# Optimization experiments

Measured on AMD Instinct MI355X. Metric: run time of the kernel, lower is better.

Reference implementation:

```python
import jax, jax.numpy as jnp
import numpy as np
import math

B, S, D, H = 4, 2048, 1024, 16
HD = D // H

def setup_inputs() -> dict:
    key = jax.random.key(0)
    ks = jax.random.split(key, 14)
    scale = 1.0 / math.sqrt(D)
    inp = {
        "q": jax.random.normal(ks[0], (B, S, D), jnp.float32),
        "k": jax.random.normal(ks[1], (B, S, D), jnp.float32),
        "v": jax.random.normal(ks[2], (B, S, D), jnp.float32),
        "time_diffs": jax.random.uniform(ks[3], (B, S, S), jnp.float32),
        "mask": jax.random.randint(ks[4], (B, 1, S, S), 0, 2, jnp.int32),
        "Wq": jax.random.normal(ks[5], (D, D), jnp.float32) * scale,
        "bq": jnp.zeros((D,), jnp.float32),
        "Wk": jax.random.normal(ks[6], (D, D), jnp.float32) * scale,
        "bk": jnp.zeros((D,), jnp.float32),
        "Wv": jax.random.normal(ks[7], (D, D), jnp.float32) * scale,
        "bv": jnp.zeros((D,), jnp.float32),
        "Wo": jax.random.normal(ks[8], (D, D), jnp.float32) * scale,
        "bo": jnp.zeros((D,), jnp.float32),
        "gamma": jnp.asarray(1.0, jnp.float32),
    }
    return inp


def reference(q, k, v, time_diffs, mask, Wq, bq, Wk, bk, Wv, bv, Wo, bo, gamma):
    # Linear projections (torch Linear: x @ W.T + b), split heads -> [B,H,S,HD]
    def proj(x, W, b):
        return (x @ W.T + b).reshape(B, S, H, HD).transpose(0, 2, 1, 3)

    qh = proj(q, Wq, bq)
    kh = proj(k, Wk, bk)
    vh = proj(v, Wv, bv)

    # [B,H,S,S] attention scores
    scores = jnp.einsum("bhqd,bhkd->bhqk", qh, kh) / math.sqrt(HD)
    # additive time-decay bias, broadcast over heads
    scores = scores + jnp.exp(-gamma * time_diffs)[:, None, :, :]
    scores = jnp.where(mask == 0, jnp.float32(-1e9), scores)

    attn = jax.nn.softmax(scores, axis=-1)
    # dropout is identity in eval mode (training=False)
    out = jnp.einsum("bhqk,bhkd->bhqd", attn, vh)
    out = out.transpose(0, 2, 1, 3).reshape(B, S, D)
    return out @ Wo.T + bo
```

## Files before the change

### kernel.cpp

```cpp
#include <hip/hip_runtime.h>
#include <hip/hip_bf16.h>

#define B_ 4
#define S_ 2048
#define D_ 1024
#define H_ 16
#define M_ 8192

typedef __attribute__((ext_vector_type(8))) _Float16 h8;
typedef __attribute__((ext_vector_type(4))) _Float16 h4;
typedef __attribute__((ext_vector_type(8))) short    s8;
typedef __attribute__((ext_vector_type(4))) float    f4;

#define AS1(p) ((const __attribute__((address_space(1))) void*)(p))
#define AS3(p) ((__attribute__((address_space(3))) void*)(p))

__device__ __forceinline__ f4 mfma16(h8 a, h8 b, f4 c) {
  return __builtin_amdgcn_mfma_f32_16x16x32_f16(a, b, c, 0, 0, 0);
}

struct CastArgs {
  const float* src[7];
  _Float16*    dst[7];
  int cum[8];
};

__global__ __launch_bounds__(256) void cast_kernel(CastArgs a) {
  int idx = blockIdx.x * 256 + threadIdx.x;
  if (idx >= a.cum[7]) return;
  int seg = 0;
#pragma unroll
  for (int s = 1; s < 7; ++s) seg += (idx >= a.cum[s]) ? 1 : 0;
  size_t off = (size_t)(idx - a.cum[seg]) * 8;
  const float4* sp = (const float4*)(a.src[seg] + off);
  float4 u = sp[0], v = sp[1];
  union { _Float16 h[8]; h8 v8; } o;
  o.h[0] = (_Float16)u.x; o.h[1] = (_Float16)u.y;
  o.h[2] = (_Float16)u.z; o.h[3] = (_Float16)u.w;
  o.h[4] = (_Float16)v.x; o.h[5] = (_Float16)v.y;
  o.h[6] = (_Float16)v.z; o.h[7] = (_Float16)v.w;
  *(h8*)(a.dst[seg] + off) = o.v8;
}

__global__ __launch_bounds__(256) void bias_kernel(
    const float* __restrict__ td, const int* __restrict__ mask,
    const float* __restrict__ gptr, _Float16* __restrict__ biasT)
{
  __shared__ _Float16 tile[64][66];
  const float gamma = gptr[0];
  const int bid = blockIdx.x;
  const int b  = bid >> 10;
  const int i0 = ((bid >> 5) & 31) * 64;
  const int j0 = (bid & 31) * 64;
  const int t = threadIdx.x;
  const int c = t & 63, r0 = t >> 6;
#pragma unroll
  for (int it = 0; it < 16; ++it) {
    int r = r0 * 16 + it;
    size_t off = ((size_t)b * S_ + i0 + r) * S_ + j0 + c;
    float tv = td[off];
    int mk = mask[off];
    tile[r][c] = mk ? (_Float16)(__expf(-gamma * tv) * 1.4426950408889634f)
                    : (_Float16)(-30000.0f);
  }
  __syncthreads();
#pragma unroll
  for (int it = 0; it < 16; ++it) {
    int r = r0 * 16 + it;
    biasT[((size_t)b * S_ + j0 + r) * S_ + i0 + c] = tile[c][r];
  }
}

template<bool F32OUT>
__global__ __launch_bounds__(256, 3) void gemm_bt(
    const _Float16* __restrict__ A,
    const _Float16* __restrict__ Bt,
    const float*    __restrict__ bias,
    void*           __restrict__ Cout,
    float scale)
{
  __shared__ __align__(16) _Float16 Alds[128 * 64];
  __shared__ __align__(16) _Float16 Blds[128 * 64];
  const int t = threadIdx.x;
  const int lane = t & 63, w = t >> 6;
  const int wm = w >> 1, wn = w & 1;
  const int m0 = blockIdx.x * 128, n0 = blockIdx.y * 128;
  const int ll = lane & 15, lg = lane >> 4;
  f4 acc[4][4] = {};

  for (int kt = 0; kt < 1024; kt += 64) {
    __syncthreads();
#pragma unroll
    for (int i = 0; i < 4; ++i) {
      int slot = i * 256 + t;
      int r = slot >> 3;
      int gs = ((slot & 7) ^ (r & 7)) * 8;
      __builtin_amdgcn_global_load_lds(AS1(A  + (size_t)(m0 + r) * 1024 + kt + gs),
                                       AS3((char*)Alds + (i * 256 + w * 64) * 16), 16, 0, 0);
      __builtin_amdgcn_global_load_lds(AS1(Bt + (size_t)(n0 + r) * 1024 + kt + gs),
                                       AS3((char*)Blds + (i * 256 + w * 64) * 16), 16, 0, 0);
    }
    __syncthreads();
#pragma unroll
    for (int ks = 0; ks < 2; ++ks) {
      h8 af[4], bf[4];
#pragma unroll
      for (int im = 0; im < 4; ++im) {
        int R = wm * 64 + im * 16 + ll;
        af[im] = *(const h8*)((const char*)Alds + R * 128 + (((ks * 4 + lg) ^ (R & 7)) << 4));
      }
#pragma unroll
      for (int in = 0; in < 4; ++in) {
        int R = wn * 64 + in * 16 + ll;
        bf[in] = *(const h8*)((const char*)Blds + R * 128 + (((ks * 4 + lg) ^ (R & 7)) << 4));
      }
#pragma unroll
      for (int im = 0; im < 4; ++im)
#pragma unroll
        for (int in = 0; in < 4; ++in)
          acc[im][in] = mfma16(af[im], bf[in], acc[im][in]);
    }
  }
#pragma unroll
  for (int im = 0; im < 4; ++im)
#pragma unroll
    for (int in = 0; in < 4; ++in) {
      int col = n0 + wn * 64 + in * 16 + ll;
      float bv = bias[col];
#pragma unroll
      for (int r = 0; r < 4; ++r) {
        int row = m0 + wm * 64 + im * 16 + lg * 4 + r;
        float vv = (acc[im][in][r] + bv) * scale;
        if constexpr (F32OUT) ((float*)Cout)[(size_t)row * 1024 + col] = vv;
        else ((_Float16*)Cout)[(size_t)row * 1024 + col] = (_Float16)vv;
      }
    }
}

__global__ __launch_bounds__(256) void transpose_v(
    const _Float16* __restrict__ Vp, _Float16* __restrict__ Vt)
{
  __shared__ __align__(16) short tile[64][72];
  const int blk = blockIdx.x;
  const int b = blk >> 9, h = (blk >> 5) & 15, st = blk & 31;
  const int s0 = st * 64, t = threadIdx.x;
#pragma unroll
  for (int it = 0; it < 2; ++it) {
    int slot = it * 256 + t;
    int r = slot >> 3, c = slot & 7;
    s8 v = *(const s8*)(Vp + (size_t)(b * S_ + s0 + r) * D_ + h * 64 + c * 8);
    *(s8*)&tile[r][c * 8] = v;
  }
  __syncthreads();
#pragma unroll
  for (int it = 0; it < 2; ++it) {
    int slot = it * 256 + t;
    int hd = slot >> 3, c = slot & 7;
    union { short hh[8]; s8 v8; } o;
#pragma unroll
    for (int e = 0; e < 8; ++e) o.hh[e] = tile[c * 8 + e][hd];
    *(s8*)(Vt + (size_t)((b * 16 + h) * 64 + hd) * S_ + s0 + c * 8) = o.v8;
  }
}

#define KL_OFF   0
#define VL_OFF   16384
#define PL_OFF   32768

__global__ __launch_bounds__(256, 4) void attn_kernel(
    const _Float16* __restrict__ Qp,
    const _Float16* __restrict__ Kp,
    const _Float16* __restrict__ Vt,
    const _Float16* __restrict__ biasT,
    _Float16*       __restrict__ Oa)
{
  __shared__ __align__(16) char lds[40960];
  const int t = threadIdx.x;
  const int lane = t & 63, w = t >> 6;
  const int ll = lane & 15, lg = lane >> 4;
  const int bid = blockIdx.x;
  const int b  = bid >> 9;
  const int h  = (bid >> 5) & 15;
  const int qg = bid & 31;
  const int q0 = qg * 64 + w * 16;

  const int lrow = lane >> 3;
  const int lcs  = (lane & 7) ^ lrow;

  const _Float16* Kg = Kp + (size_t)b * S_ * D_ + h * 64;
  const _Float16* Vg = Vt + (size_t)(b * 16 + h) * 64 * S_;
  const _Float16* Bg = biasT + (size_t)b * S_ * S_ + q0 + lg * 4;

  char* pbase = lds + PL_OFF + w * 2048;

  const size_t qrow = (size_t)(b * S_ + q0 + ll) * D_ + h * 64;
  h8 qf0 = *(const h8*)(Qp + qrow + lg * 8);
  h8 qf1 = *(const h8*)(Qp + qrow + 32 + lg * 8);

  float lsum[4] = {0.f, 0.f, 0.f, 0.f};
  f4 accO[4] = {};

  auto STAGE = [&](int kt, int bufb) {
#pragma unroll
    for (int j = 0; j < 4; ++j) {
      int i = w * 4 + j;
      int g = i & 7;
      int row8 = g * 8 + lrow;
      const _Float16* src;
      char* dst;
      if (i < 8) {
        src = Kg + (size_t)(kt + row8) * D_ + lcs * 8;
        dst = lds + KL_OFF + bufb * 8192 + g * 1024;
      } else {
        src = Vg + (size_t)row8 * S_ + kt + lcs * 8;
        dst = lds + VL_OFF + bufb * 8192 + g * 1024;
      }
      __builtin_amdgcn_global_load_lds(AS1(src), AS3(dst), 16, 0, 0);
    }
  };
  auto BLOAD = [&](int kt, h4 (&dst)[4]) {
#pragma unroll
    for (int jf = 0; jf < 4; ++jf)
      dst[jf] = *(const h4*)(Bg + (size_t)(kt + 16 * jf + ll) * S_);
  };

  h4 bcur[4], bnext[4];

  STAGE(0, 0);
  BLOAD(0, bcur);
  asm volatile("s_waitcnt vmcnt(0)" ::: "memory");
  __builtin_amdgcn_sched_barrier(0);
  __builtin_amdgcn_s_barrier();
  __builtin_amdgcn_sched_barrier(0);

  for (int tt = 0; tt < 32; ++tt) {
    const int bufb = tt & 1;
    if (tt < 31) {
      STAGE((tt + 1) * 64, bufb ^ 1);
      BLOAD((tt + 1) * 64, bnext);
      asm volatile("s_waitcnt vmcnt(12)" ::: "memory");
    } else {
      asm volatile("s_waitcnt vmcnt(0)" ::: "memory");
    }
    __builtin_amdgcn_sched_barrier(0);
    __builtin_amdgcn_s_barrier();
    __builtin_amdgcn_sched_barrier(0);

    const char* Kb = lds + KL_OFF + bufb * 8192;
    const char* Vb = lds + VL_OFF + bufb * 8192;

    f4 accS[4] = {};
#pragma unroll
    for (int jf = 0; jf < 4; ++jf) {
      int row = jf * 16 + ll;
      h8 k0 = *(const h8*)(Kb + row * 128 + (((lg)     ^ (row & 7)) << 4));
      h8 k1 = *(const h8*)(Kb + row * 128 + (((4 + lg) ^ (row & 7)) << 4));
      accS[jf] = mfma16(qf0, k0, accS[jf]);
      accS[jf] = mfma16(qf1, k1, accS[jf]);
    }

#pragma unroll
    for (int jf = 0; jf < 4; ++jf)
#pragma unroll
      for (int r = 0; r < 4; ++r) {
        float sc = accS[jf][r] + (float)bcur[jf][r];
        float p;
        asm("v_exp_f32 %0, %1" : "=v"(p) : "v"(sc));
        lsum[r] += p;
        int i = lg * 4 + r, j = ll + 16 * jf;
        *(_Float16*)(pbase + i * 128 + ((2 * j) ^ ((i & 7) << 4))) = (_Float16)p;
      }
#pragma unroll
    for (int jf = 0; jf < 4; ++jf) bcur[jf] = bnext[jf];

#pragma unroll
    for (int ks = 0; ks < 2; ++ks) {
      h8 pf = *(const h8*)(pbase + ll * 128 + ((ks * 64 + lg * 16) ^ ((ll & 7) << 4)));
#pragma unroll
      for (int df = 0; df < 4; ++df) {
        int vrow = df * 16 + ll;
        h8 vfr = *(const h8*)(Vb + vrow * 128 + (((ks * 4 + lg) ^ (vrow & 7)) << 4));
        accO[df] = mfma16(vfr, pf, accO[df]);
      }
    }

    __builtin_amdgcn_sched_barrier(0);
    __builtin_amdgcn_s_barrier();
    __builtin_amdgcn_sched_barrier(0);
  }

#pragma unroll
  for (int d = 1; d < 16; d <<= 1)
#pragma unroll
    for (int r = 0; r < 4; ++r)
      lsum[r] += __shfl_xor(lsum[r], d);

  float ls = lsum[0];
  ls = ((ll & 3) == 1) ? lsum[1] : ls;
  ls = ((ll & 3) == 2) ? lsum[2] : ls;
  ls = ((ll & 3) == 3) ? lsum[3] : ls;
  float lf = __shfl(ls, ((ll >> 2) << 4) + ll);
  float linv = 1.0f / lf;
#pragma unroll
  for (int df = 0; df < 4; ++df)
#pragma unroll
    for (int r = 0; r < 4; ++r) {
      size_t orow = (size_t)(b * S_ + q0 + ll) * D_ + h * 64 + df * 16 + lg * 4 + r;
      Oa[orow] = (_Float16)(accO[df][r] * linv);
    }
}

extern "C" void kernel_launch(void* const* d_in, const int* in_sizes, int n_in,
                              void* d_out, int out_size, void* d_ws, size_t ws_size,
                              hipStream_t stream) {
  const float* q    = (const float*)d_in[0];
  const float* k    = (const float*)d_in[1];
  const float* v    = (const float*)d_in[2];
  const float* td   = (const float*)d_in[3];
  const int*   mask = (const int*)d_in[4];
  const float* Wq   = (const float*)d_in[5];
  const float* bq   = (const float*)d_in[6];
  const float* Wk   = (const float*)d_in[7];
  const float* bk   = (const float*)d_in[8];
  const float* Wv   = (const float*)d_in[9];
  const float* bv   = (const float*)d_in[10];
  const float* Wo   = (const float*)d_in[11];
  const float* bo   = (const float*)d_in[12];
  const float* gm   = (const float*)d_in[13];

  const size_t MD = (size_t)M_ * D_;
  const size_t WW = (size_t)D_ * D_;
  if (ws_size < (8 * MD + 4 * WW) * sizeof(_Float16)) return;

  _Float16* base = (_Float16*)d_ws;
  _Float16* qh = base;
  _Float16* kh = qh + MD;
  _Float16* vh = kh + MD;
  _Float16* wq = vh + MD;
  _Float16* wk = wq + WW;
  _Float16* wv = wk + WW;
  _Float16* wo = wv + WW;
  _Float16* Qp = wo + WW;
  _Float16* Kp = Qp + MD;
  _Float16* Vp = Kp + MD;
  _Float16* Vt = Vp + MD;
  _Float16* Oa = Vt + MD;
  _Float16* biasT = qh;

  CastArgs ca;
  ca.src[0] = q;  ca.src[1] = k;  ca.src[2] = v;
  ca.src[3] = Wq; ca.src[4] = Wk; ca.src[5] = Wv; ca.src[6] = Wo;
  ca.dst[0] = qh; ca.dst[1] = kh; ca.dst[2] = vh;
  ca.dst[3] = wq; ca.dst[4] = wk; ca.dst[5] = wv; ca.dst[6] = wo;
  int sizes[7] = {(int)(MD / 8), (int)(MD / 8), (int)(MD / 8),
                  (int)(WW / 8), (int)(WW / 8), (int)(WW / 8), (int)(WW / 8)};
  int c = 0; ca.cum[0] = 0;
  for (int i = 0; i < 7; ++i) { c += sizes[i]; ca.cum[i + 1] = c; }
  cast_kernel<<<(c + 255) / 256, 256, 0, stream>>>(ca);

  dim3 gg(64, 8);
  gemm_bt<false><<<gg, 256, 0, stream>>>(qh, wq, bq, Qp, 0.18033688011112042f);
  gemm_bt<false><<<gg, 256, 0, stream>>>(kh, wk, bk, Kp, 1.0f);
  bias_kernel<<<4096, 256, 0, stream>>>(td, mask, gm, biasT);
  gemm_bt<false><<<gg, 256, 0, stream>>>(vh, wv, bv, Vp, 1.0f);
  transpose_v<<<2048, 256, 0, stream>>>(Vp, Vt);
  attn_kernel<<<2048, 256, 0, stream>>>(Qp, Kp, Vt, biasT, Oa);
  gemm_bt<true><<<gg, 256, 0, stream>>>(Oa, wo, bo, d_out, 1.0f);
}
```

Measured before the change: 348.8 us.

## Compute transposed scores so bias stays row-major; drop bias transpose kernel tiling

The S=QK^T MFMA is swapped to produce S^T fragments, so each lane owns one query row and the bias can be read in natural row-major layout. That lets the bias kernel become a simple vectorized elementwise pass with no LDS transpose. The bias is preloaded into the MFMA accumulator, the P store becomes packed 8-byte writes, and the row-sum reduction shrinks to two shuffles. Loads for the next tile are now issued after the QK MFMAs, relying on __syncthreads for ordering, with the loop unrolled by two to ping-pong bias registers.

```diff
diff --git a/kernel.cpp b/kernel.cpp
--- a/kernel.cpp
+++ b/kernel.cpp
@@ -9,6 +9,7 @@
 
 typedef __attribute__((ext_vector_type(8))) _Float16 h8;
 typedef __attribute__((ext_vector_type(4))) _Float16 h4;
+typedef __attribute__((ext_vector_type(2))) __fp16   fp16x2;
 typedef __attribute__((ext_vector_type(8))) short    s8;
 typedef __attribute__((ext_vector_type(4))) float    f4;
 
@@ -44,31 +45,25 @@
 
 __global__ __launch_bounds__(256) void bias_kernel(
     const float* __restrict__ td, const int* __restrict__ mask,
-    const float* __restrict__ gptr, _Float16* __restrict__ biasT)
+    const float* __restrict__ gptr, _Float16* __restrict__ biasN)
 {
-  __shared__ _Float16 tile[64][66];
   const float gamma = gptr[0];
-  const int bid = blockIdx.x;
-  const int b  = bid >> 10;
-  const int i0 = ((bid >> 5) & 31) * 64;
-  const int j0 = (bid & 31) * 64;
-  const int t = threadIdx.x;
-  const int c = t & 63, r0 = t >> 6;
-#pragma unroll
-  for (int it = 0; it < 16; ++it) {
-    int r = r0 * 16 + it;
-    size_t off = ((size_t)b * S_ + i0 + r) * S_ + j0 + c;
-    float tv = td[off];
-    int mk = mask[off];
-    tile[r][c] = mk ? (_Float16)(__expf(-gamma * tv) * 1.4426950408889634f)
-                    : (_Float16)(-30000.0f);
-  }
-  __syncthreads();
-#pragma unroll
-  for (int it = 0; it < 16; ++it) {
-    int r = r0 * 16 + it;
-    biasT[((size_t)b * S_ + j0 + r) * S_ + i0 + c] = tile[c][r];
-  }
+  size_t idx = (size_t)blockIdx.x * 256 + threadIdx.x;
+  size_t off = idx * 8;
+  const float4* tp = (const float4*)(td + off);
+  const int4*   mp = (const int4*)(mask + off);
+  float4 t0 = tp[0], t1 = tp[1];
+  int4   m0 = mp[0], m1 = mp[1];
+  union { _Float16 h[8]; h8 v8; } o;
+  o.h[0] = m0.x ? (_Float16)(__expf(-gamma * t0.x) * 1.4426950408889634f) : (_Float16)(-30000.0f);
+  o.h[1] = m0.y ? (_Float16)(__expf(-gamma * t0.y) * 1.4426950408889634f) : (_Float16)(-30000.0f);
+  o.h[2] = m0.z ? (_Float16)(__expf(-gamma * t0.z) * 1.4426950408889634f) : (_Float16)(-30000.0f);
+  o.h[3] = m0.w ? (_Float16)(__expf(-gamma * t0.w) * 1.4426950408889634f) : (_Float16)(-30000.0f);
+  o.h[4] = m1.x ? (_Float16)(__expf(-gamma * t1.x) * 1.4426950408889634f) : (_Float16)(-30000.0f);
+  o.h[5] = m1.y ? (_Float16)(__expf(-gamma * t1.y) * 1.4426950408889634f) : (_Float16)(-30000.0f);
+  o.h[6] = m1.z ? (_Float16)(__expf(-gamma * t1.z) * 1.4426950408889634f) : (_Float16)(-30000.0f);
+  o.h[7] = m1.w ? (_Float16)(__expf(-gamma * t1.w) * 1.4426950408889634f) : (_Float16)(-30000.0f);
+  *(h8*)(biasN + off) = o.v8;
 }
 
 template<bool F32OUT>
@@ -171,7 +166,7 @@
     const _Float16* __restrict__ Qp,
     const _Float16* __restrict__ Kp,
     const _Float16* __restrict__ Vt,
-    const _Float16* __restrict__ biasT,
+    const _Float16* __restrict__ biasN,
     _Float16*       __restrict__ Oa)
 {
   __shared__ __align__(16) char lds[40960];
@@ -189,7 +184,7 @@
 
   const _Float16* Kg = Kp + (size_t)b * S_ * D_ + h * 64;
   const _Float16* Vg = Vt + (size_t)(b * 16 + h) * 64 * S_;
-  const _Float16* Bg = biasT + (size_t)b * S_ * S_ + q0 + lg * 4;
+  const _Float16* Bg = biasN + ((size_t)b * S_ + q0 + ll) * S_;
 
   char* pbase = lds + PL_OFF + w * 2048;
 
@@ -197,7 +192,7 @@
   h8 qf0 = *(const h8*)(Qp + qrow + lg * 8);
   h8 qf1 = *(const h8*)(Qp + qrow + 32 + lg * 8);
 
-  float lsum[4] = {0.f, 0.f, 0.f, 0.f};
+  float lsum = 0.f;
   f4 accO[4] = {};
 
   auto STAGE = [&](int kt, int bufb) {
@@ -221,57 +216,49 @@
   auto BLOAD = [&](int kt, h4 (&dst)[4]) {
 #pragma unroll
     for (int jf = 0; jf < 4; ++jf)
-      dst[jf] = *(const h4*)(Bg + (size_t)(kt + 16 * jf + ll) * S_);
+      dst[jf] = *(const h4*)(Bg + kt + 16 * jf + lg * 4);
   };
 
-  h4 bcur[4], bnext[4];
-
-  STAGE(0, 0);
-  BLOAD(0, bcur);
-  asm volatile("s_waitcnt vmcnt(0)" ::: "memory");
-  __builtin_amdgcn_sched_barrier(0);
-  __builtin_amdgcn_s_barrier();
-  __builtin_amdgcn_sched_barrier(0);
-
-  for (int tt = 0; tt < 32; ++tt) {
+  auto BODY = [&](int tt, h4 (&bc)[4], h4 (&bn)[4]) {
     const int bufb = tt & 1;
-    if (tt < 31) {
-      STAGE((tt + 1) * 64, bufb ^ 1);
-      BLOAD((tt + 1) * 64, bnext);
-      asm volatile("s_waitcnt vmcnt(12)" ::: "memory");
-    } else {
-      asm volatile("s_waitcnt vmcnt(0)" ::: "memory");
-    }
-    __builtin_amdgcn_sched_barrier(0);
-    __builtin_amdgcn_s_barrier();
-    __builtin_amdgcn_sched_barrier(0);
-
     const char* Kb = lds + KL_OFF + bufb * 8192;
     const char* Vb = lds + VL_OFF + bufb * 8192;
 
-    f4 accS[4] = {};
+    f4 accS[4];
+#pragma unroll
+    for (int jf = 0; jf < 4; ++jf) {
+      accS[jf][0] = (float)bc[jf][0];
+      accS[jf][1] = (float)bc[jf][1];
+      accS[jf][2] = (float)bc[jf][2];
+      accS[jf][3] = (float)bc[jf][3];
+    }
 #pragma unroll
     for (int jf = 0; jf < 4; ++jf) {
       int row = jf * 16 + ll;
       h8 k0 = *(const h8*)(Kb + row * 128 + (((lg)     ^ (row & 7)) << 4));
       h8 k1 = *(const h8*)(Kb + row * 128 + (((4 + lg) ^ (row & 7)) << 4));
-      accS[jf] = mfma16(qf0, k0, accS[jf]);
-      accS[jf] = mfma16(qf1, k1, accS[jf]);
-    }
-
-#pragma unroll
-    for (int jf = 0; jf < 4; ++jf)
-#pragma unroll
-      for (int r = 0; r < 4; ++r) {
-        float sc = accS[jf][r] + (float)bcur[jf][r];
-        float p;
-        asm("v_exp_f32 %0, %1" : "=v"(p) : "v"(sc));
-        lsum[r] += p;
-        int i = lg * 4 + r, j = ll + 16 * jf;
-        *(_Float16*)(pbase + i * 128 + ((2 * j) ^ ((i & 7) << 4))) = (_Float16)p;
-      }
-#pragma unroll
-    for (int jf = 0; jf < 4; ++jf) bcur[jf] = bnext[jf];
+      accS[jf] = mfma16(k0, qf0, accS[jf]);
+      accS[jf] = mfma16(k1, qf1, accS[jf]);
+    }
+
+    if (tt < 31) {
+      STAGE((tt + 1) * 64, bufb ^ 1);
+      BLOAD((tt + 1) * 64, bn);
+    }
+
+#pragma unroll
+    for (int jf = 0; jf < 4; ++jf) {
+      float p0, p1, p2, p3;
+      asm("v_exp_f32 %0, %1" : "=v"(p0) : "v"(accS[jf][0]));
+      asm("v_exp_f32 %0, %1" : "=v"(p1) : "v"(accS[jf][1]));
+      asm("v_exp_f32 %0, %1" : "=v"(p2) : "v"(accS[jf][2]));
+      asm("v_exp_f32 %0, %1" : "=v"(p3) : "v"(accS[jf][3]));
+      lsum += (p0 + p1) + (p2 + p3);
+      union { fp16x2 h[2]; unsigned long long u; } wv;
+      wv.h[0] = __builtin_amdgcn_cvt_pkrtz(p0, p1);
+      wv.h[1] = __builtin_amdgcn_cvt_pkrtz(p2, p3);
+      *(unsigned long long*)(pbase + ll * 128 + ((32 * jf + 8 * lg) ^ ((ll & 7) << 4))) = wv.u;
+    }
 
 #pragma unroll
     for (int ks = 0; ks < 2; ++ks) {
@@ -284,23 +271,23 @@
       }
     }
 
-    __builtin_amdgcn_sched_barrier(0);
-    __builtin_amdgcn_s_barrier();
-    __builtin_amdgcn_sched_barrier(0);
+    __syncthreads();
+  };
+
+  h4 bA[4], bB[4];
+
+  STAGE(0, 0);
+  BLOAD(0, bA);
+  __syncthreads();
+
+  for (int tt = 0; tt < 32; tt += 2) {
+    BODY(tt,     bA, bB);
+    BODY(tt + 1, bB, bA);
   }
 
-#pragma unroll
-  for (int d = 1; d < 16; d <<= 1)
-#pragma unroll
-    for (int r = 0; r < 4; ++r)
-      lsum[r] += __shfl_xor(lsum[r], d);
-
-  float ls = lsum[0];
-  ls = ((ll & 3) == 1) ? lsum[1] : ls;
-  ls = ((ll & 3) == 2) ? lsum[2] : ls;
-  ls = ((ll & 3) == 3) ? lsum[3] : ls;
-  float lf = __shfl(ls, ((ll >> 2) << 4) + ll);
-  float linv = 1.0f / lf;
+  lsum += __shfl_xor(lsum, 16);
+  lsum += __shfl_xor(lsum, 32);
+  float linv = 1.0f / lsum;
 #pragma unroll
   for (int df = 0; df < 4; ++df)
 #pragma unroll
@@ -345,7 +332,7 @@
   _Float16* Vp = Kp + MD;
   _Float16* Vt = Vp + MD;
   _Float16* Oa = Vt + MD;
-  _Float16* biasT = qh;
+  _Float16* biasN = qh;
 
   CastArgs ca;
   ca.src[0] = q;  ca.src[1] = k;  ca.src[2] = v;
@@ -361,9 +348,9 @@
   dim3 gg(64, 8);
   gemm_bt<false><<<gg, 256, 0, stream>>>(qh, wq, bq, Qp, 0.18033688011112042f);
   gemm_bt<false><<<gg, 256, 0, stream>>>(kh, wk, bk, Kp, 1.0f);
-  bias_kernel<<<4096, 256, 0, stream>>>(td, mask, gm, biasT);
+  bias_kernel<<<8192, 256, 0, stream>>>(td, mask, gm, biasN);
   gemm_bt<false><<<gg, 256, 0, stream>>>(vh, wv, bv, Vp, 1.0f);
   transpose_v<<<2048, 256, 0, stream>>>(Vp, Vt);
-  attn_kernel<<<2048, 256, 0, stream>>>(Qp, Kp, Vt, biasT, Oa);
+  attn_kernel<<<2048, 256, 0, stream>>>(Qp, Kp, Vt, biasN, Oa);
   gemm_bt<true><<<gg, 256, 0, stream>>>(Oa, wo, bo, d_out, 1.0f);
 }
```

Measured after the change: 325.3 us. 6.8% less time.
